# Performance work log

Hardware: AMD Instinct MI355X
Metric: run time of the kernel (lower is better)

## Reference

```python
import jax, jax.numpy as jnp
import numpy as np

WAY = 64
SHOT = 16
D = 768
NQ = 2048
REG = 0.5  # reg_param from __init__


def setup_inputs() -> dict:
    key = jax.random.key(0)
    k1, k2, k3, k4 = jax.random.split(key, 4)
    support_X = jax.random.normal(k1, (WAY * SHOT, D), jnp.float32)
    query_X = jax.random.normal(k2, (NQ, D), jnp.float32)
    labels = (jnp.arange(WAY * SHOT) // SHOT).astype(jnp.int32)  # shot per class, sorted
    m = 0.01 * jax.random.normal(k3, (1, D), jnp.float32)
    kappa = jnp.float32(0.1)
    nu = jnp.float32(D)
    triu_diag = jnp.ones((D,), jnp.float32)
    triu_lower = jnp.eye(D, dtype=jnp.float32) + 0.01 * jax.random.normal(k4, (D, D), jnp.float32)
    return {
        'support_X': support_X, 'query_X': query_X, 'm': m, 'kappa': kappa,
        'nu': nu, 'triu_diag': triu_diag, 'triu_lower': triu_lower,
        'labels': labels, 'way': WAY,
    }


def _metaqda_fb(support_X, query_X, m, kappa, nu, triu_diag, triu_lower, labels, way):
    d = support_X.shape[1]
    f = support_X.dtype
    kappa_ = jnp.abs(kappa) + 1e-6
    nu_ = jnp.clip(nu, d - 1 + 1e-6)
    # Cholesky-factor prior: diag(|triu_diag|) + strictly-lower part of triu_lower
    strict_lower = jnp.tril(jnp.ones((d, d), f), -1)
    L = jnp.diag(jnp.abs(triu_diag)) + triu_lower * strict_lower
    # Segment reductions over classes via one-hot (labels cover 0..way-1)
    onehot = (labels[:, None] == jnp.arange(way)[None, :]).astype(f)  # [N, C]
    Nc = onehot.sum(0)                                                # [C]
    means = (onehot.T @ support_X) / Nc[:, None]                      # [C, D]
    mu = (kappa_ / (kappa_ + Nc))[:, None] * m + (Nc / (kappa_ + Nc))[:, None] * means  # [C, D]
    # Per-class sum of outer products: S_c = X_c^T X_c  (fused segment outer-product sum)
    S = jnp.einsum('nc,nd,ne->cde', onehot, support_X, support_X)     # [C, D, D]
    prior = L @ L.T + kappa_ * (m.T @ m)                              # [D, D]
    sigma_ns = prior[None] + S - (kappa_ + Nc)[:, None, None] * jnp.einsum('cd,ce->cde', mu, mu)
    scale = (kappa_ + Nc + 1.0) / ((nu_ + Nc - d + 1.0) * (kappa_ + Nc))
    sigma = sigma_ns * scale[:, None, None]                           # [C, D, D]
    sigma_inv = (1.0 - REG) * jnp.linalg.inv(sigma) + REG * jnp.eye(d, dtype=f)
    _, logdet = jnp.linalg.slogdet(sigma)                             # [C]
    common = nu_ + Nc + 1.0 - d                                       # [C]
    bias = (jax.lax.lgamma(0.5 * (common + d)) - jax.lax.lgamma(0.5 * common)
            - 0.5 * d * jnp.log(common) - 0.5 * logdet)               # [C]
    # Batched Mahalanobis quadratic form over all (query, class) pairs
    diff = query_X[:, None, :] - mu[None]                             # [Q, C, D]
    dist = jnp.einsum('qcd,cde,qce->qc', diff, sigma_inv, diff)       # [Q, C]
    return bias[None, :] - 0.5 * (common + d)[None, :] * jnp.log1p(dist / common[None, :])


def reference(support_X, query_X, m, kappa, nu, triu_diag, triu_lower, labels, way):
    return _metaqda_fb(support_X, query_X, m, kappa, nu, triu_diag, triu_lower, labels, way)
```

## Files before the change

### kernel.cpp

```cpp
#include <hip/hip_runtime.h>
#include <hip/hip_bf16.h>
#include <math.h>

constexpr int DD   = 768;
constexpr int NSUP = 1024;
constexpr int NQQ  = 2048;
constexpr int NC   = 64;
constexpr int SHOT = 16;
constexpr int RR   = 18;
constexpr float REGP = 0.5f;
constexpr int DDS = DD * DD;
constexpr int NROWS = NQQ + NSUP + 1 + NC;
constexpr int TRB  = 16;
constexpr int NTB  = (NROWS + TRB - 1) / TRB;
constexpr int NDB  = DD / 64;
constexpr int LW   = 384;
constexpr int LB   = LW / 64;

__global__ __launch_bounds__(256) void build_L(const float* __restrict__ tdiag,
                                               const float* __restrict__ tlow,
                                               float* __restrict__ Lm) {
    int idx = blockIdx.x * 256 + threadIdx.x;
    if (idx >= DDS) return;
    int i = idx / DD, j = idx % DD;
    float v = (i == j) ? fabsf(tdiag[i]) : (i > j ? tlow[idx] : 0.f);
    Lm[idx] = v;
}

__global__ __launch_bounds__(256) void class_stats(const float* __restrict__ Xs,
                                                   const float* __restrict__ m,
                                                   const int* __restrict__ labels,
                                                   const float* __restrict__ kappa,
                                                   float* __restrict__ mmu,
                                                   int* __restrict__ cls_idx,
                                                   int* __restrict__ cls_n) {
    int c = blockIdx.x;
    __shared__ int lidx[SHOT];
    __shared__ int lcount;
    if (threadIdx.x == 0) lcount = 0;
    __syncthreads();
    for (int n = threadIdx.x; n < NSUP; n += 256) {
        if (labels[n] == c) {
            int pos = atomicAdd(&lcount, 1);
            if (pos < SHOT) lidx[pos] = n;
        }
    }
    __syncthreads();
    int cnt = lcount < SHOT ? lcount : SHOT;
    if (threadIdx.x < SHOT) cls_idx[c * SHOT + threadIdx.x] = (threadIdx.x < cnt) ? lidx[threadIdx.x] : 0;
    if (threadIdx.x == 0) cls_n[c] = cnt;
    float kap = fabsf(kappa[0]) + 1e-6f;
    float fn = (float)cnt;
    float wm = kap / (kap + fn);
    float wx = 1.f / (kap + fn);
    if (c == 0) {
        for (int d = threadIdx.x; d < DD; d += 256) mmu[d] = m[d];
    }
    for (int d = threadIdx.x; d < DD; d += 256) {
        float s = 0.f;
        for (int t = 0; t < cnt; ++t) s += Xs[(size_t)lidx[t] * DD + d];
        mmu[(size_t)(1 + c) * DD + d] = wm * m[d] + wx * s;
    }
}

__global__ __launch_bounds__(64) void diag_inv64(const float* __restrict__ Lm,
                                                 float* __restrict__ DinvT) {
    int b = blockIdx.x;
    __shared__ float lt[64][65];
    __shared__ float xt[64][65];
    int tid = threadIdx.x;
    for (int i = 0; i < 64; ++i) {
        lt[i][tid] = Lm[(size_t)(b * 64 + i) * DD + b * 64 + tid];
        xt[i][tid] = 0.f;
    }
    __syncthreads();
    int j = tid;
    xt[j][j] = 1.f / lt[j][j];
    for (int i = j + 1; i < 64; ++i) {
        float s = 0.f;
        for (int k = j; k < i; ++k) s += lt[i][k] * xt[k][j];
        xt[i][j] = -s / lt[i][i];
    }
    __syncthreads();
    for (int t = tid; t < 4096; t += 64)
        DinvT[(size_t)b * 4096 + t] = xt[t & 63][t >> 6];
}

__global__ __launch_bounds__(256) void copy_stack(const float* __restrict__ Qx,
                                                  const float* __restrict__ Xs,
                                                  const float* __restrict__ mmu,
                                                  float* __restrict__ Trows) {
    int f = blockIdx.x * 256 + threadIdx.x;
    if (f >= NROWS * (DD / 4)) return;
    int q = f / (DD / 4);
    int d4 = f % (DD / 4);
    const float* src;
    if (q < NQQ) src = Qx + (size_t)q * DD;
    else if (q < NQQ + NSUP) src = Xs + (size_t)(q - NQQ) * DD;
    else src = mmu + (size_t)(q - NQQ - NSUP) * DD;
    float4 v = *(const float4*)(src + d4 * 4);
    *(float4*)(Trows + (size_t)q * DD + d4 * 4) = v;
}

__global__ __launch_bounds__(256) void leaf_trsm(float* __restrict__ Trows,
                                                 const float* __restrict__ Lm,
                                                 const float* __restrict__ DinvT,
                                                 int c0) {
    __shared__ float Ylds[LW * 17];
    __shared__ float Lc[64][65];
    __shared__ float Ssh[64 * 17];
    int tid = threadIdx.x;
    int a = tid & 63;
    int g = tid >> 6;
    int q0 = blockIdx.x * TRB;
    int qrow[4];
    bool valid[4];
#pragma unroll
    for (int j = 0; j < 4; ++j) {
        int q = q0 + g * 4 + j;
        valid[j] = q < NROWS;
        qrow[j] = valid[j] ? q : 0;
    }
    int db0 = c0 >> 6;

    for (int r = 0; r < LB; ++r) {
        int r0 = r * 64;
        int gcol = c0 + r0;
        float s0 = 0.f, s1 = 0.f, s2 = 0.f, s3 = 0.f;
        for (int kb = 0; kb < r; ++kb) {
            for (int t = tid; t < 4096; t += 256) {
                int i = t >> 6, k = t & 63;
                Lc[i][k] = Lm[(size_t)(gcol + i) * DD + c0 + kb * 64 + k];
            }
            __syncthreads();
            const float* ybase = &Ylds[(kb * 64) * 17 + g * 4];
#pragma unroll 16
            for (int kk = 0; kk < 64; ++kk) {
                float lv = Lc[a][kk];
                const float* yr = ybase + kk * 17;
                s0 += lv * yr[0]; s1 += lv * yr[1];
                s2 += lv * yr[2]; s3 += lv * yr[3];
            }
            __syncthreads();
        }
        Ssh[a * 17 + g * 4 + 0] = (valid[0] ? Trows[(size_t)qrow[0] * DD + gcol + a] : 0.f) - s0;
        Ssh[a * 17 + g * 4 + 1] = (valid[1] ? Trows[(size_t)qrow[1] * DD + gcol + a] : 0.f) - s1;
        Ssh[a * 17 + g * 4 + 2] = (valid[2] ? Trows[(size_t)qrow[2] * DD + gcol + a] : 0.f) - s2;
        Ssh[a * 17 + g * 4 + 3] = (valid[3] ? Trows[(size_t)qrow[3] * DD + gcol + a] : 0.f) - s3;
        __syncthreads();
        float o0 = 0.f, o1 = 0.f, o2 = 0.f, o3 = 0.f;
        const float* dptr = DinvT + (size_t)(db0 + r) * 4096 + a;
#pragma unroll 8
        for (int m = 0; m < 64; ++m) {
            float dv = dptr[m * 64];
            const float* tr = &Ssh[m * 17 + g * 4];
            o0 += dv * tr[0]; o1 += dv * tr[1];
            o2 += dv * tr[2]; o3 += dv * tr[3];
        }
        __syncthreads();
        Ylds[(r0 + a) * 17 + g * 4 + 0] = o0;
        Ylds[(r0 + a) * 17 + g * 4 + 1] = o1;
        Ylds[(r0 + a) * 17 + g * 4 + 2] = o2;
        Ylds[(r0 + a) * 17 + g * 4 + 3] = o3;
        if (valid[0]) Trows[(size_t)qrow[0] * DD + gcol + a] = o0;
        if (valid[1]) Trows[(size_t)qrow[1] * DD + gcol + a] = o1;
        if (valid[2]) Trows[(size_t)qrow[2] * DD + gcol + a] = o2;
        if (valid[3]) Trows[(size_t)qrow[3] * DD + gcol + a] = o3;
        __syncthreads();
    }
}

template <int SPLIT, bool NEG>
__global__ __launch_bounds__(256) void gemm_nt(const float* __restrict__ A0,
                                               const float* __restrict__ B,
                                               float* __restrict__ Cc,
                                               int M, int Nn, int K,
                                               int lda, int ldb, int ldc) {
    __shared__ __align__(16) float As[32][68];
    __shared__ __align__(16) float Bs[32][68];
    int bm = blockIdx.x, bn = blockIdx.y, bz = blockIdx.z;
    int row0 = bm * 64, col0 = bn * 64;
    int tid = threadIdx.x;
    int tr = tid >> 4, tc = tid & 15;
    float acc[4][4] = {};
    int nch = K >> 5;
    int klo = 32 * ((bz * nch) / SPLIT);
    int khi = 32 * (((bz + 1) * nch) / SPLIT);
    for (int k0 = klo; k0 < khi; k0 += 32) {
        for (int t = tid; t < 64 * 32; t += 256) {
            int r = t >> 5, kk = t & 31;
            int ar = row0 + r;
            As[kk][r] = (ar < M) ? A0[(size_t)ar * lda + k0 + kk] : 0.f;
            int br = col0 + r;
            Bs[kk][r] = (br < Nn) ? B[(size_t)br * ldb + k0 + kk] : 0.f;
        }
        __syncthreads();
#pragma unroll
        for (int kk = 0; kk < 32; ++kk) {
            float4 av = *(const float4*)(&As[kk][tr << 2]);
            float4 bv = *(const float4*)(&Bs[kk][tc << 2]);
            float a[4] = {av.x, av.y, av.z, av.w};
            float b[4] = {bv.x, bv.y, bv.z, bv.w};
#pragma unroll
            for (int x = 0; x < 4; ++x)
#pragma unroll
                for (int y = 0; y < 4; ++y) acc[x][y] += a[x] * b[y];
        }
        __syncthreads();
    }
#pragma unroll
    for (int x = 0; x < 4; ++x) {
        int r = row0 + tr * 4 + x;
        if (r >= M) continue;
#pragma unroll
        for (int y = 0; y < 4; ++y) {
            int cc2 = col0 + tc * 4 + y;
            if (cc2 < Nn) atomicAdd(&Cc[(size_t)r * ldc + cc2], NEG ? -acc[x][y] : acc[x][y]);
        }
    }
}

__global__ __launch_bounds__(256) void build_V(const float* __restrict__ Trows,
                                               const int* __restrict__ cls_idx,
                                               const int* __restrict__ cls_n,
                                               const float* __restrict__ kappa,
                                               float* __restrict__ Vt) {
    int row = blockIdx.x;
    int c = row / RR, i = row % RR;
    int cnt = cls_n[c];
    float kap = fabsf(kappa[0]) + 1e-6f;
    size_t srow;
    float sc = 1.f;
    if (i < SHOT) {
        if (i >= cnt) {
            for (int d = threadIdx.x; d < DD; d += 256) Vt[(size_t)row * DD + d] = 0.f;
            return;
        }
        srow = (size_t)NQQ + cls_idx[c * SHOT + i];
    } else if (i == SHOT) {
        srow = NQQ + NSUP;
        sc = sqrtf(kap);
    } else {
        srow = (size_t)NQQ + NSUP + 1 + c;
        sc = sqrtf(kap + (float)cnt);
    }
    for (int d = threadIdx.x; d < DD; d += 256)
        Vt[(size_t)row * DD + d] = sc * Trows[srow * DD + d];
}

__global__ __launch_bounds__(256) void build_M(const float* __restrict__ Trows,
                                               const float* __restrict__ mmu,
                                               const float* __restrict__ Vt,
                                               const float* __restrict__ tdiag,
                                               const float* __restrict__ kappa,
                                               const float* __restrict__ nu,
                                               const int* __restrict__ cls_n,
                                               float* __restrict__ consts,
                                               float* __restrict__ hbuf,
                                               float* __restrict__ MinvO) {
    int c = blockIdx.x;
    __shared__ double Md[RR][RR];
    __shared__ double aug[RR][2 * RR];
    __shared__ double colk[RR];
    __shared__ double red[4];
    __shared__ double gj_logdet;
    __shared__ float hs[RR];
    __shared__ float ng2t_s, mu2_s;
    int tid = threadIdx.x;
    int wave = tid >> 6, lane = tid & 63;
    const float* Vc = Vt + (size_t)c * RR * DD;
    const float* Tmu = Trows + (size_t)(NQQ + NSUP + 1 + c) * DD;
    const float* mu_raw = mmu + (size_t)(1 + c) * DD;

    for (int p = wave; p < RR * RR + RR + 2; p += 4) {
        const float *va, *vb;
        if (p < RR * RR) {
            int i = p / RR, j = p % RR;
            if (i > j) continue;
            va = Vc + (size_t)i * DD; vb = Vc + (size_t)j * DD;
        } else if (p < RR * RR + RR) {
            va = Vc + (size_t)(p - RR * RR) * DD; vb = Tmu;
        } else if (p == RR * RR + RR) {
            va = Tmu; vb = Tmu;
        } else {
            va = mu_raw; vb = mu_raw;
        }
        double s = 0.0;
        for (int d = lane; d < DD; d += 64) s += (double)va[d] * (double)vb[d];
        for (int off = 32; off; off >>= 1) s += __shfl_down(s, off);
        if (lane == 0) {
            if (p < RR * RR) { int i = p / RR, j = p % RR; Md[i][j] = s; Md[j][i] = s; }
            else if (p < RR * RR + RR) hs[p - RR * RR] = (float)s;
            else if (p == RR * RR + RR) ng2t_s = (float)s;
            else mu2_s = (float)s;
        }
    }
    double sl = 0.0;
    for (int k = tid; k < DD; k += 256) sl += log((double)fabsf(tdiag[k]));
    for (int off = 32; off; off >>= 1) sl += __shfl_down(sl, off);
    if (lane == 0) red[wave] = sl;
    __syncthreads();

    if (tid == 0) {
        for (int i = 0; i < RR - 1; ++i) Md[i][i] += 1.0;
        Md[RR - 1][RR - 1] -= 1.0;
        gj_logdet = 0.0;
    }
    __syncthreads();
    for (int t = tid; t < RR * 2 * RR; t += 256) {
        int r2 = t / (2 * RR), j2 = t % (2 * RR);
        aug[r2][j2] = (j2 < RR) ? Md[r2][j2] : ((j2 - RR == r2) ? 1.0 : 0.0);
    }
    __syncthreads();
    for (int k = 0; k < RR; ++k) {
        if (tid == 0) {
            int piv = k; double best = fabs(aug[k][k]);
            for (int r2 = k + 1; r2 < RR; ++r2) {
                double v = fabs(aug[r2][k]);
                if (v > best) { best = v; piv = r2; }
            }
            if (piv != k) {
                for (int j2 = 0; j2 < 2 * RR; ++j2) {
                    double tmp = aug[k][j2]; aug[k][j2] = aug[piv][j2]; aug[piv][j2] = tmp;
                }
            }
            double pv = aug[k][k];
            gj_logdet += log(fabs(pv));
            double inv = 1.0 / pv;
            for (int j2 = 0; j2 < 2 * RR; ++j2) aug[k][j2] *= inv;
        }
        __syncthreads();
        if (tid < RR) colk[tid] = (tid == k) ? 0.0 : aug[tid][k];
        __syncthreads();
        for (int t = tid; t < RR * 2 * RR; t += 256) {
            int r2 = t / (2 * RR), j2 = t % (2 * RR);
            if (r2 != k) aug[r2][j2] -= colk[r2] * aug[k][j2];
        }
        __syncthreads();
    }
    if (tid == 0) {
        double sumlog = red[0] + red[1] + red[2] + red[3];
        double kap = fabs((double)kappa[0]) + 1e-6;
        double nu_ = fmax((double)nu[0], (double)(DD - 1) + 1e-6);
        double fn = (double)cls_n[c];
        double common = nu_ + fn + 1.0 - (double)DD;
        double scale = (kap + fn + 1.0) / (common * (kap + fn));
        double logdet_sigma = (double)DD * log(scale) + 2.0 * sumlog + gj_logdet;
        double bias = lgamma(0.5 * (common + DD)) - lgamma(0.5 * common)
                    - 0.5 * DD * log(common) - 0.5 * logdet_sigma;
        consts[c * 8 + 0] = (float)((1.0 - (double)REGP) / scale);
        consts[c * 8 + 1] = (float)common;
        consts[c * 8 + 2] = (float)(0.5 * (common + DD));
        consts[c * 8 + 3] = (float)bias;
        consts[c * 8 + 4] = (float)(1.0 / sqrt(kap + fn));
        consts[c * 8 + 5] = ng2t_s;
        consts[c * 8 + 6] = mu2_s;
        consts[c * 8 + 7] = 0.f;
    }
    __syncthreads();
    for (int t = tid; t < RR * RR; t += 256)
        MinvO[(size_t)c * RR * RR + t] = (float)aug[t / RR][RR + t % RR];
    if (tid < RR) hbuf[c * RR + tid] = hs[tid];
}

__global__ __launch_bounds__(256) void query_norms(const float* __restrict__ Qx,
                                                   const float* __restrict__ Trows,
                                                   float* __restrict__ q2,
                                                   float* __restrict__ nq2t) {
    int q = blockIdx.x * 4 + (threadIdx.x >> 6);
    int lane = threadIdx.x & 63;
    float s1 = 0.f, s2 = 0.f;
    for (int d = lane; d < DD; d += 64) {
        float a = Qx[(size_t)q * DD + d]; s1 += a * a;
        float b = Trows[(size_t)q * DD + d]; s2 += b * b;
    }
    for (int off = 32; off; off >>= 1) { s1 += __shfl_down(s1, off); s2 += __shfl_down(s2, off); }
    if (lane == 0) { q2[q] = s1; nq2t[q] = s2; }
}

__global__ __launch_bounds__(256) void final_kernel(const float* __restrict__ P,
                                                    const float* __restrict__ dotqmu,
                                                    const float* __restrict__ q2,
                                                    const float* __restrict__ nq2t,
                                                    const float* __restrict__ consts,
                                                    const float* __restrict__ hbuf,
                                                    const float* __restrict__ Minv,
                                                    float* __restrict__ out) {
    int c = blockIdx.x, qt = blockIdx.y;
    __shared__ float Ms[RR][RR];
    __shared__ float hlds[RR];
    __shared__ float cs[8];
    int tid = threadIdx.x;
    for (int t = tid; t < RR * RR; t += 256) Ms[t / RR][t % RR] = Minv[(size_t)c * RR * RR + t];
    if (tid < RR) hlds[tid] = hbuf[c * RR + tid];
    if (tid < 8) cs[tid] = consts[c * 8 + tid];
    __syncthreads();
    int q = qt * 256 + tid;
    const float* Pq = P + (size_t)q * (NC * RR) + c * RR;
    float p[RR];
    float p17raw = Pq[RR - 1];
#pragma unroll
    for (int i = 0; i < RR; ++i) p[i] = Pq[i] - hlds[i];
    float quad = 0.f;
#pragma unroll
    for (int i = 0; i < RR; ++i) {
        float t = 0.f;
#pragma unroll
        for (int j = 0; j < RR; ++j) t += Ms[i][j] * p[j];
        quad += p[i] * t;
    }
    float w1 = cs[0], common = cs[1], coef = cs[2], bias = cs[3];
    float inv_s17 = cs[4], ng2t = cs[5], mu2 = cs[6];
    float Gu2 = nq2t[q] - 2.f * p17raw * inv_s17 + ng2t;
    float u2 = q2[q] - 2.f * dotqmu[(size_t)q * NC + c] + mu2;
    float dist = w1 * (Gu2 - quad) + REGP * u2;
    out[(size_t)q * NC + c] = bias - coef * log1pf(dist / common);
}

extern "C" void kernel_launch(void* const* d_in, const int* in_sizes, int n_in,
                              void* d_out, int out_size, void* d_ws, size_t ws_size,
                              hipStream_t stream) {
    const float* Xs    = (const float*)d_in[0];
    const float* Qx    = (const float*)d_in[1];
    const float* m     = (const float*)d_in[2];
    const float* kappa = (const float*)d_in[3];
    const float* nu    = (const float*)d_in[4];
    const float* tdiag = (const float*)d_in[5];
    const float* tlow  = (const float*)d_in[6];
    const int* labels  = (const int*)d_in[7];
    float* out = (float*)d_out;

    float* ws = (float*)d_ws;
    float* Lm     = ws;
    float* mmu    = Lm + DDS;
    float* DinvT  = mmu + (size_t)(NC + 1) * DD;
    float* Trows  = DinvT + (size_t)NDB * 64 * 64;
    float* Vt     = Trows + (size_t)NROWS * DD;
    float* P      = Vt + (size_t)NC * RR * DD;
    float* dotqmu = P + (size_t)NQQ * NC * RR;
    float* q2     = dotqmu + (size_t)NQQ * NC;
    float* nq2t   = q2 + NQQ;
    float* consts = nq2t + NQQ;
    float* hbuf   = consts + NC * 8;
    float* MinvB  = hbuf + NC * RR;
    int* cls_idx  = (int*)(MinvB + (size_t)NC * RR * RR);
    int* cls_n    = cls_idx + NC * SHOT;

    hipMemsetAsync(P, 0, ((size_t)NQQ * NC * RR + (size_t)NQQ * NC) * sizeof(float), stream);

    build_L<<<(DDS + 255) / 256, 256, 0, stream>>>(tdiag, tlow, Lm);
    class_stats<<<NC, 256, 0, stream>>>(Xs, m, labels, kappa, mmu, cls_idx, cls_n);
    diag_inv64<<<NDB, 64, 0, stream>>>(Lm, DinvT);
    copy_stack<<<(NROWS * (DD / 4) + 255) / 256, 256, 0, stream>>>(Qx, Xs, mmu, Trows);
    leaf_trsm<<<NTB, 256, 0, stream>>>(Trows, Lm, DinvT, 0);
    gemm_nt<2, true><<<dim3((NROWS + 63) / 64, LW / 64, 2), 256, 0, stream>>>(
        Trows, Lm + (size_t)LW * DD, Trows + LW, NROWS, LW, LW, DD, DD, DD);
    leaf_trsm<<<NTB, 256, 0, stream>>>(Trows, Lm, DinvT, LW);
    build_V<<<NC * RR, 256, 0, stream>>>(Trows, cls_idx, cls_n, kappa, Vt);
    build_M<<<NC, 256, 0, stream>>>(Trows, mmu, Vt, tdiag, kappa, nu, cls_n, consts, hbuf, MinvB);
    query_norms<<<NQQ / 4, 256, 0, stream>>>(Qx, Trows, q2, nq2t);
    gemm_nt<3, false><<<dim3(NQQ / 64, (NC * RR) / 64, 3), 256, 0, stream>>>(
        Trows, Vt, P, NQQ, NC * RR, DD, DD, DD, NC * RR);
    gemm_nt<4, false><<<dim3(NQQ / 64, 1, 4), 256, 0, stream>>>(
        Qx, mmu + DD, dotqmu, NQQ, NC, DD, DD, DD, NC);
    final_kernel<<<dim3(NC, NQQ / 256), 256, 0, stream>>>(P, dotqmu, q2, nq2t, consts, hbuf, MinvB, out);
}
```

Baseline: 647.7 us.

## Shrink TRSM row tile, use 128-row GEMM tiles, transpose projection outputs

The leaf triangular solve now gives each 64-thread group a single row (4 rows per block instead of 16). This raises block count for parallelism but means each L tile load is reused across fewer rows. The GEMM becomes a 128x64 tile variant with 8x4 register blocking, cutting L/Vt re-reads per output. The projection GEMMs now write class-major transposed outputs (PT, dotqmuT) with a smaller K-split, so final_kernel reads coalesced along queries.

```diff
diff --git a/kernel.cpp b/kernel.cpp
--- a/kernel.cpp
+++ b/kernel.cpp
@@ -11,7 +11,7 @@
 constexpr float REGP = 0.5f;
 constexpr int DDS = DD * DD;
 constexpr int NROWS = NQQ + NSUP + 1 + NC;
-constexpr int TRB  = 16;
+constexpr int TRB  = 4;
 constexpr int NTB  = (NROWS + TRB - 1) / TRB;
 constexpr int NDB  = DD / 64;
 constexpr int LW   = 384;
@@ -106,111 +106,91 @@
                                                  const float* __restrict__ Lm,
                                                  const float* __restrict__ DinvT,
                                                  int c0) {
-    __shared__ float Ylds[LW * 17];
+    __shared__ float Ylds[LW * 5];
     __shared__ float Lc[64][65];
-    __shared__ float Ssh[64 * 17];
+    __shared__ float Ssh[64 * 5];
     int tid = threadIdx.x;
     int a = tid & 63;
     int g = tid >> 6;
-    int q0 = blockIdx.x * TRB;
-    int qrow[4];
-    bool valid[4];
-#pragma unroll
-    for (int j = 0; j < 4; ++j) {
-        int q = q0 + g * 4 + j;
-        valid[j] = q < NROWS;
-        qrow[j] = valid[j] ? q : 0;
-    }
+    int q = blockIdx.x * TRB + g;
+    bool valid = q < NROWS;
+    int qq = valid ? q : 0;
     int db0 = c0 >> 6;
 
     for (int r = 0; r < LB; ++r) {
         int r0 = r * 64;
         int gcol = c0 + r0;
-        float s0 = 0.f, s1 = 0.f, s2 = 0.f, s3 = 0.f;
+        float s = 0.f;
         for (int kb = 0; kb < r; ++kb) {
             for (int t = tid; t < 4096; t += 256) {
                 int i = t >> 6, k = t & 63;
                 Lc[i][k] = Lm[(size_t)(gcol + i) * DD + c0 + kb * 64 + k];
             }
             __syncthreads();
-            const float* ybase = &Ylds[(kb * 64) * 17 + g * 4];
+            const float* ybase = &Ylds[(kb * 64) * 5 + g];
 #pragma unroll 16
-            for (int kk = 0; kk < 64; ++kk) {
-                float lv = Lc[a][kk];
-                const float* yr = ybase + kk * 17;
-                s0 += lv * yr[0]; s1 += lv * yr[1];
-                s2 += lv * yr[2]; s3 += lv * yr[3];
-            }
+            for (int kk = 0; kk < 64; ++kk)
+                s += Lc[a][kk] * ybase[kk * 5];
             __syncthreads();
         }
-        Ssh[a * 17 + g * 4 + 0] = (valid[0] ? Trows[(size_t)qrow[0] * DD + gcol + a] : 0.f) - s0;
-        Ssh[a * 17 + g * 4 + 1] = (valid[1] ? Trows[(size_t)qrow[1] * DD + gcol + a] : 0.f) - s1;
-        Ssh[a * 17 + g * 4 + 2] = (valid[2] ? Trows[(size_t)qrow[2] * DD + gcol + a] : 0.f) - s2;
-        Ssh[a * 17 + g * 4 + 3] = (valid[3] ? Trows[(size_t)qrow[3] * DD + gcol + a] : 0.f) - s3;
-        __syncthreads();
-        float o0 = 0.f, o1 = 0.f, o2 = 0.f, o3 = 0.f;
+        Ssh[a * 5 + g] = (valid ? Trows[(size_t)qq * DD + gcol + a] : 0.f) - s;
+        __syncthreads();
+        float o = 0.f;
         const float* dptr = DinvT + (size_t)(db0 + r) * 4096 + a;
 #pragma unroll 8
-        for (int m = 0; m < 64; ++m) {
-            float dv = dptr[m * 64];
-            const float* tr = &Ssh[m * 17 + g * 4];
-            o0 += dv * tr[0]; o1 += dv * tr[1];
-            o2 += dv * tr[2]; o3 += dv * tr[3];
-        }
-        __syncthreads();
-        Ylds[(r0 + a) * 17 + g * 4 + 0] = o0;
-        Ylds[(r0 + a) * 17 + g * 4 + 1] = o1;
-        Ylds[(r0 + a) * 17 + g * 4 + 2] = o2;
-        Ylds[(r0 + a) * 17 + g * 4 + 3] = o3;
-        if (valid[0]) Trows[(size_t)qrow[0] * DD + gcol + a] = o0;
-        if (valid[1]) Trows[(size_t)qrow[1] * DD + gcol + a] = o1;
-        if (valid[2]) Trows[(size_t)qrow[2] * DD + gcol + a] = o2;
-        if (valid[3]) Trows[(size_t)qrow[3] * DD + gcol + a] = o3;
+        for (int m = 0; m < 64; ++m)
+            o += dptr[m * 64] * Ssh[m * 5 + g];
+        Ylds[(r0 + a) * 5 + g] = o;
+        if (valid) Trows[(size_t)qq * DD + gcol + a] = o;
         __syncthreads();
     }
 }
 
 template <int SPLIT, bool NEG>
-__global__ __launch_bounds__(256) void gemm_nt(const float* __restrict__ A0,
-                                               const float* __restrict__ B,
-                                               float* __restrict__ Cc,
-                                               int M, int Nn, int K,
-                                               int lda, int ldb, int ldc) {
-    __shared__ __align__(16) float As[32][68];
+__global__ __launch_bounds__(256) void gemm_nt128(const float* __restrict__ A0,
+                                                  const float* __restrict__ B,
+                                                  float* __restrict__ Cc,
+                                                  int M, int Nn, int K,
+                                                  int lda, int ldb, int ldc) {
+    __shared__ __align__(16) float As[32][132];
     __shared__ __align__(16) float Bs[32][68];
     int bm = blockIdx.x, bn = blockIdx.y, bz = blockIdx.z;
-    int row0 = bm * 64, col0 = bn * 64;
+    int row0 = bm * 128, col0 = bn * 64;
     int tid = threadIdx.x;
     int tr = tid >> 4, tc = tid & 15;
-    float acc[4][4] = {};
+    float acc[8][4] = {};
     int nch = K >> 5;
     int klo = 32 * ((bz * nch) / SPLIT);
     int khi = 32 * (((bz + 1) * nch) / SPLIT);
     for (int k0 = klo; k0 < khi; k0 += 32) {
-        for (int t = tid; t < 64 * 32; t += 256) {
+        for (int t = tid; t < 128 * 32; t += 256) {
             int r = t >> 5, kk = t & 31;
             int ar = row0 + r;
             As[kk][r] = (ar < M) ? A0[(size_t)ar * lda + k0 + kk] : 0.f;
+        }
+        for (int t = tid; t < 64 * 32; t += 256) {
+            int r = t >> 5, kk = t & 31;
             int br = col0 + r;
             Bs[kk][r] = (br < Nn) ? B[(size_t)br * ldb + k0 + kk] : 0.f;
         }
         __syncthreads();
 #pragma unroll
         for (int kk = 0; kk < 32; ++kk) {
-            float4 av = *(const float4*)(&As[kk][tr << 2]);
-            float4 bv = *(const float4*)(&Bs[kk][tc << 2]);
-            float a[4] = {av.x, av.y, av.z, av.w};
+            float4 a0v = *(const float4*)(&As[kk][tr * 8]);
+            float4 a1v = *(const float4*)(&As[kk][tr * 8 + 4]);
+            float4 bv  = *(const float4*)(&Bs[kk][tc * 4]);
+            float a[8] = {a0v.x, a0v.y, a0v.z, a0v.w, a1v.x, a1v.y, a1v.z, a1v.w};
             float b[4] = {bv.x, bv.y, bv.z, bv.w};
 #pragma unroll
-            for (int x = 0; x < 4; ++x)
+            for (int x = 0; x < 8; ++x)
 #pragma unroll
                 for (int y = 0; y < 4; ++y) acc[x][y] += a[x] * b[y];
         }
         __syncthreads();
     }
 #pragma unroll
-    for (int x = 0; x < 4; ++x) {
-        int r = row0 + tr * 4 + x;
+    for (int x = 0; x < 8; ++x) {
+        int r = row0 + tr * 8 + x;
         if (r >= M) continue;
 #pragma unroll
         for (int y = 0; y < 4; ++y) {
@@ -378,8 +358,8 @@
     if (lane == 0) { q2[q] = s1; nq2t[q] = s2; }
 }
 
-__global__ __launch_bounds__(256) void final_kernel(const float* __restrict__ P,
-                                                    const float* __restrict__ dotqmu,
+__global__ __launch_bounds__(256) void final_kernel(const float* __restrict__ PT,
+                                                    const float* __restrict__ dotqmuT,
                                                     const float* __restrict__ q2,
                                                     const float* __restrict__ nq2t,
                                                     const float* __restrict__ consts,
@@ -396,11 +376,11 @@
     if (tid < 8) cs[tid] = consts[c * 8 + tid];
     __syncthreads();
     int q = qt * 256 + tid;
-    const float* Pq = P + (size_t)q * (NC * RR) + c * RR;
+    const float* Pc = PT + (size_t)c * RR * NQQ + q;
     float p[RR];
-    float p17raw = Pq[RR - 1];
-#pragma unroll
-    for (int i = 0; i < RR; ++i) p[i] = Pq[i] - hlds[i];
+    float p17raw = Pc[(size_t)(RR - 1) * NQQ];
+#pragma unroll
+    for (int i = 0; i < RR; ++i) p[i] = Pc[(size_t)i * NQQ] - hlds[i];
     float quad = 0.f;
 #pragma unroll
     for (int i = 0; i < RR; ++i) {
@@ -412,7 +392,7 @@
     float w1 = cs[0], common = cs[1], coef = cs[2], bias = cs[3];
     float inv_s17 = cs[4], ng2t = cs[5], mu2 = cs[6];
     float Gu2 = nq2t[q] - 2.f * p17raw * inv_s17 + ng2t;
-    float u2 = q2[q] - 2.f * dotqmu[(size_t)q * NC + c] + mu2;
+    float u2 = q2[q] - 2.f * dotqmuT[(size_t)c * NQQ + q] + mu2;
     float dist = w1 * (Gu2 - quad) + REGP * u2;
     out[(size_t)q * NC + c] = bias - coef * log1pf(dist / common);
 }
@@ -431,37 +411,37 @@
     float* out = (float*)d_out;
 
     float* ws = (float*)d_ws;
-    float* Lm     = ws;
-    float* mmu    = Lm + DDS;
-    float* DinvT  = mmu + (size_t)(NC + 1) * DD;
-    float* Trows  = DinvT + (size_t)NDB * 64 * 64;
-    float* Vt     = Trows + (size_t)NROWS * DD;
-    float* P      = Vt + (size_t)NC * RR * DD;
-    float* dotqmu = P + (size_t)NQQ * NC * RR;
-    float* q2     = dotqmu + (size_t)NQQ * NC;
-    float* nq2t   = q2 + NQQ;
-    float* consts = nq2t + NQQ;
-    float* hbuf   = consts + NC * 8;
-    float* MinvB  = hbuf + NC * RR;
-    int* cls_idx  = (int*)(MinvB + (size_t)NC * RR * RR);
-    int* cls_n    = cls_idx + NC * SHOT;
-
-    hipMemsetAsync(P, 0, ((size_t)NQQ * NC * RR + (size_t)NQQ * NC) * sizeof(float), stream);
+    float* Lm      = ws;
+    float* mmu     = Lm + DDS;
+    float* DinvT   = mmu + (size_t)(NC + 1) * DD;
+    float* Trows   = DinvT + (size_t)NDB * 64 * 64;
+    float* Vt      = Trows + (size_t)NROWS * DD;
+    float* PT      = Vt + (size_t)NC * RR * DD;
+    float* dotqmuT = PT + (size_t)NC * RR * NQQ;
+    float* q2      = dotqmuT + (size_t)NC * NQQ;
+    float* nq2t    = q2 + NQQ;
+    float* consts  = nq2t + NQQ;
+    float* hbuf    = consts + NC * 8;
+    float* MinvB   = hbuf + NC * RR;
+    int* cls_idx   = (int*)(MinvB + (size_t)NC * RR * RR);
+    int* cls_n     = cls_idx + NC * SHOT;
+
+    hipMemsetAsync(PT, 0, ((size_t)NC * RR * NQQ + (size_t)NC * NQQ) * sizeof(float), stream);
 
     build_L<<<(DDS + 255) / 256, 256, 0, stream>>>(tdiag, tlow, Lm);
     class_stats<<<NC, 256, 0, stream>>>(Xs, m, labels, kappa, mmu, cls_idx, cls_n);
     diag_inv64<<<NDB, 64, 0, stream>>>(Lm, DinvT);
     copy_stack<<<(NROWS * (DD / 4) + 255) / 256, 256, 0, stream>>>(Qx, Xs, mmu, Trows);
     leaf_trsm<<<NTB, 256, 0, stream>>>(Trows, Lm, DinvT, 0);
-    gemm_nt<2, true><<<dim3((NROWS + 63) / 64, LW / 64, 2), 256, 0, stream>>>(
+    gemm_nt128<2, true><<<dim3((NROWS + 127) / 128, LW / 64, 2), 256, 0, stream>>>(
         Trows, Lm + (size_t)LW * DD, Trows + LW, NROWS, LW, LW, DD, DD, DD);
     leaf_trsm<<<NTB, 256, 0, stream>>>(Trows, Lm, DinvT, LW);
     build_V<<<NC * RR, 256, 0, stream>>>(Trows, cls_idx, cls_n, kappa, Vt);
     build_M<<<NC, 256, 0, stream>>>(Trows, mmu, Vt, tdiag, kappa, nu, cls_n, consts, hbuf, MinvB);
     query_norms<<<NQQ / 4, 256, 0, stream>>>(Qx, Trows, q2, nq2t);
-    gemm_nt<3, false><<<dim3(NQQ / 64, (NC * RR) / 64, 3), 256, 0, stream>>>(
-        Trows, Vt, P, NQQ, NC * RR, DD, DD, DD, NC * RR);
-    gemm_nt<4, false><<<dim3(NQQ / 64, 1, 4), 256, 0, stream>>>(
-        Qx, mmu + DD, dotqmu, NQQ, NC, DD, DD, DD, NC);
-    final_kernel<<<dim3(NC, NQQ / 256), 256, 0, stream>>>(P, dotqmu, q2, nq2t, consts, hbuf, MinvB, out);
-}
+    gemm_nt128<2, false><<<dim3((NC * RR) / 128, NQQ / 64, 2), 256, 0, stream>>>(
+        Vt, Trows, PT, NC * RR, NQQ, DD, DD, DD, NQQ);
+    gemm_nt128<4, false><<<dim3(1, NQQ / 64, 4), 256, 0, stream>>>(
+        mmu + DD, Qx, dotqmuT, NC, NQQ, DD, DD, DD, NQQ);
+    final_kernel<<<dim3(NC, NQQ / 256), 256, 0, stream>>>(PT, dotqmuT, q2, nq2t, consts, hbuf, MinvB, out);
+}
```

After: 697.0 us. 7.6% more time.
